# Kernel optimization log

Measured on AMD Instinct MI355X. Metric: run time of the kernel, lower is better.

The kernel has to match this reference:

```python
import jax, jax.numpy as jnp
import numpy as np

N = 200_000          # total nodes
C = 256              # in_channels
B = 64               # batch_size (num graphs)
NPG = N // B         # nodes per graph = max_num_nodes = 3125
E = 3_200_000        # edges (avg degree 16)
RATIO = 0.5
MULTIPLIER = 1.0


def setup_inputs() -> dict:
    key = jax.random.key(0)
    k1, k2, k3, k4, k5, k6 = jax.random.split(key, 6)
    x = jax.random.normal(k1, (N, C), dtype=jnp.float32)
    # hk.initializers.TruncatedNormal() ~ truncated normal, stddev 1
    p = jax.random.truncated_normal(k2, -2.0, 2.0, (C,), dtype=jnp.float32)
    # edges constrained within each graph (realistic graph batching)
    g = jax.random.randint(k3, (E,), 0, B, dtype=jnp.int32)
    senders = g * NPG + jax.random.randint(k4, (E,), 0, NPG, dtype=jnp.int32)
    receivers = g * NPG + jax.random.randint(k5, (E,), 0, NPG, dtype=jnp.int32)
    # sorted batch vector: graph id per node
    batch = jnp.arange(N, dtype=jnp.int32) // NPG
    return {"x": x, "p": p, "senders": senders, "receivers": receivers, "batch": batch}


def _segment_softmax(score, batch, num_segments):
    # batch_softmax from haiku-geometric: numerically-stable per-graph softmax
    mx = jax.ops.segment_max(score, batch, num_segments=num_segments)
    e = jnp.exp(score - mx[batch])
    denom = jax.ops.segment_sum(e, batch, num_segments=num_segments)
    return e / denom[batch]


def reference(x, p, senders, receivers, batch):
    batch_size = B
    num_nodes = x.shape[0]
    # per-node score: <x_i, p>, then softmax within each graph
    score = jnp.sum(x * p, axis=-1)                       # [N]
    score = _segment_softmax(score, batch, batch_size)    # [N]

    # select_batch_topk: keep first k nodes (by position) per graph,
    # move the rest to a new batch id == batch_size.
    nodes_per_batch = jax.ops.segment_sum(
        jnp.ones(num_nodes, dtype=jnp.int32), batch, num_segments=batch_size)
    cum_num_nodes = jnp.concatenate(
        [jnp.zeros(1, jnp.int32), jnp.cumsum(nodes_per_batch)[:-1].astype(jnp.int32)])
    # ratio < 1 branch
    k = jnp.ceil(RATIO * nodes_per_batch).astype(jnp.int32)   # [B]
    index_batch = jnp.arange(num_nodes, dtype=jnp.int32) - cum_num_nodes[batch]
    threshold_per_batch = k[batch] - 1
    new_batch = jnp.where(index_batch <= threshold_per_batch,
                          batch, jnp.full(batch.shape, batch_size, dtype=batch.dtype))

    # gate features by score (multiplier == 1 -> no extra scale)
    x_gated = x * score[:, None]

    # stable sort nodes so dropped nodes go to the end
    new_perm = jnp.argsort(new_batch)          # stable
    x_out = x_gated[new_perm]
    new_batch_sorted = new_batch[new_perm]

    # turn edges touching dropped nodes into self-loops (faithful to source,
    # including the sequential where-overwrite of senders then receivers)
    new_batch_idx = jnp.max(batch) + 1
    mask = (new_batch_sorted[senders] == new_batch_idx) | \
           (new_batch_sorted[receivers] == new_batch_idx)
    senders_out = jnp.where(mask, receivers, senders)
    receivers_out = jnp.where(mask, senders_out, receivers)
    return x_out, senders_out, receivers_out, new_batch_sorted
```

## Files before the change

### kernel.cpp

```cpp
#include <hip/hip_runtime.h>
#include <hip/hip_bf16.h>
#include <stdint.h>


#define RATIO 0.5f

typedef float f32x4 __attribute__((ext_vector_type(4)));
typedef int   i32x4 __attribute__((ext_vector_type(4)));

__global__ __launch_bounds__(256) void k_scores(
    const float* __restrict__ x, const float* __restrict__ p,
    float* __restrict__ s, int N) {
    int node = blockIdx.x * 4 + (threadIdx.x >> 6);
    int lane = threadIdx.x & 63;
    if (node >= N) return;
    const f32x4 pv = *reinterpret_cast<const f32x4*>(p + lane * 4);
    const f32x4 xv = *reinterpret_cast<const f32x4*>(x + (size_t)node * 256 + lane * 4);
    float acc = xv.x * pv.x + xv.y * pv.y + xv.z * pv.z + xv.w * pv.w;
    #pragma unroll
    for (int off = 32; off; off >>= 1) acc += __shfl_down(acc, off, 64);
    if (lane == 0) s[node] = acc;
}

__global__ __launch_bounds__(256) void k_boundary(
    const int* __restrict__ batch, int N, int* __restrict__ start) {
    int i = blockIdx.x * blockDim.x + threadIdx.x;
    if (i >= N) return;
    int b = batch[i];
    if (i == 0 || batch[i - 1] != b) start[b] = i;
}

__global__ __launch_bounds__(64) void k_meta(
    int N, int B, const int* __restrict__ start,
    int* __restrict__ kk, int* __restrict__ Kb, int* __restrict__ Db,
    int* __restrict__ Ktot) {
    int g = threadIdx.x;
    int st = start[g];
    int en = (g == B - 1) ? N : start[g + 1];
    int cnt = en - st;
    int kv = (int)ceilf(RATIO * (float)cnt);
    int dv = cnt - kv;
    int kp = kv, dp = dv;
    #pragma unroll
    for (int off = 1; off < 64; off <<= 1) {
        int a = __shfl_up(kp, off, 64);
        int b_ = __shfl_up(dp, off, 64);
        if (g >= off) { kp += a; dp += b_; }
    }
    kk[g] = kv;
    Kb[g] = kp - kv;
    Db[g] = dp - dv;
    if (g == B - 1) *Ktot = kp;
}

__global__ __launch_bounds__(256) void k_stats(
    const float* __restrict__ s, const int* __restrict__ start, int N, int B,
    float* __restrict__ mx, float* __restrict__ denom) {
    int g = blockIdx.x;
    int st = start[g];
    int en = (g == B - 1) ? N : start[g + 1];
    __shared__ float red[256];
    float m = -INFINITY;
    for (int i = st + threadIdx.x; i < en; i += 256) m = fmaxf(m, s[i]);
    red[threadIdx.x] = m; __syncthreads();
    for (int o = 128; o; o >>= 1) {
        if (threadIdx.x < o) red[threadIdx.x] = fmaxf(red[threadIdx.x], red[threadIdx.x + o]);
        __syncthreads();
    }
    m = red[0]; __syncthreads();
    float sum = 0.f;
    for (int i = st + threadIdx.x; i < en; i += 256) sum += expf(s[i] - m);
    red[threadIdx.x] = sum; __syncthreads();
    for (int o = 128; o; o >>= 1) {
        if (threadIdx.x < o) red[threadIdx.x] += red[threadIdx.x + o];
        __syncthreads();
    }
    if (threadIdx.x == 0) { mx[g] = m; denom[g] = red[0]; }
}

__global__ __launch_bounds__(256) void k_scatter(
    const float* __restrict__ x, const float* __restrict__ s,
    const int* __restrict__ batch, const int* __restrict__ start,
    const int* __restrict__ kk, const int* __restrict__ Kb, const int* __restrict__ Db,
    const int* __restrict__ Ktot, const float* __restrict__ mx, const float* __restrict__ denom,
    int N, int B, float* __restrict__ xout, float* __restrict__ nbout) {
    int node = blockIdx.x * 4 + (threadIdx.x >> 6);
    if (node >= N) return;
    int lane = threadIdx.x & 63;
    int g = batch[node];
    int idx = node - start[g];
    int kv = kk[g];
    bool kept = idx < kv;
    int pos = kept ? (Kb[g] + idx) : (*Ktot + Db[g] + (idx - kv));
    float sc = expf(s[node] - mx[g]) / denom[g];
    const f32x4 xv = *reinterpret_cast<const f32x4*>(x + (size_t)node * 256 + lane * 4);
    f32x4 o;
    o.x = xv.x * sc;
    o.y = xv.y * sc;
    o.z = xv.z * sc;
    o.w = xv.w * sc;
    __builtin_nontemporal_store(o, reinterpret_cast<f32x4*>(xout + (size_t)pos * 256 + lane * 4));
    if (lane == 0)
        __builtin_nontemporal_store((float)(kept ? g : B), nbout + pos);
}

__global__ __launch_bounds__(256) void k_edges(
    const int* __restrict__ snd, const int* __restrict__ rcv, int E,
    const int* __restrict__ Ktot,
    float* __restrict__ sout, float* __restrict__ rout) {
    int t = blockIdx.x * blockDim.x + threadIdx.x;
    int base = t * 4;
    if (base >= E) return;
    int kt = *Ktot;
    if (base + 4 <= E) {
        i32x4 s4 = __builtin_nontemporal_load(reinterpret_cast<const i32x4*>(snd + base));
        i32x4 r4 = __builtin_nontemporal_load(reinterpret_cast<const i32x4*>(rcv + base));
        f32x4 so, ro;
        so.x = (float)(((s4.x >= kt) || (r4.x >= kt)) ? r4.x : s4.x);
        so.y = (float)(((s4.y >= kt) || (r4.y >= kt)) ? r4.y : s4.y);
        so.z = (float)(((s4.z >= kt) || (r4.z >= kt)) ? r4.z : s4.z);
        so.w = (float)(((s4.w >= kt) || (r4.w >= kt)) ? r4.w : s4.w);
        ro.x = (float)r4.x;
        ro.y = (float)r4.y;
        ro.z = (float)r4.z;
        ro.w = (float)r4.w;
        __builtin_nontemporal_store(so, reinterpret_cast<f32x4*>(sout + base));
        __builtin_nontemporal_store(ro, reinterpret_cast<f32x4*>(rout + base));
    } else {
        for (int e = base; e < E; ++e) {
            int sv = snd[e], rv = rcv[e];
            bool m = (sv >= kt) || (rv >= kt);
            sout[e] = (float)(m ? rv : sv);
            rout[e] = (float)rv;
        }
    }
}

extern "C" void kernel_launch(void* const* d_in, const int* in_sizes, int n_in,
                              void* d_out, int out_size, void* d_ws, size_t ws_size,
                              hipStream_t stream) {
    const float* x = (const float*)d_in[0];
    const float* p = (const float*)d_in[1];
    const int* senders = (const int*)d_in[2];
    const int* receivers = (const int*)d_in[3];
    const int* batch = (const int*)d_in[4];

    const int C = in_sizes[1];
    const int E = in_sizes[2];
    const int N = in_sizes[4];
    const int B = 64;

    char* ws = (char*)d_ws;
    float* s   = (float*)ws;
    int* start = (int*)(ws + (size_t)N * 4);
    int* kk    = start + B;
    int* Kb    = kk + B;
    int* Db    = Kb + B;
    int* Ktot  = Db + B;
    float* mx    = (float*)(Ktot + 1);
    float* denom = mx + B;

    float* out   = (float*)d_out;
    float* xout  = out;
    float* sout  = out + (size_t)N * C;
    float* rout  = sout + E;
    float* nbout = rout + E;

    k_scores  <<<(N + 3) / 4, 256, 0, stream>>>(x, p, s, N);
    k_boundary<<<(N + 255) / 256, 256, 0, stream>>>(batch, N, start);
    k_meta    <<<1, 64, 0, stream>>>(N, B, start, kk, Kb, Db, Ktot);
    k_stats   <<<B, 256, 0, stream>>>(s, start, N, B, mx, denom);
    k_scatter <<<(N + 3) / 4, 256, 0, stream>>>(x, s, batch, start, kk, Kb, Db, Ktot,
                                                mx, denom, N, B, xout, nbout);
    k_edges   <<<(E + 1023) / 1024, 256, 0, stream>>>(senders, receivers, E, Ktot, sout, rout);
}
```

Baseline: 125.9 us.

## Fuse six kernels into three: scores+boundary, meta+stats, scatter+edges

Folds the graph-boundary detection into the score kernel and runs the prefix-sum metadata as an extra block of the softmax-stats kernel. The edge-remap work is piggybacked onto every estride-th block of the feature scatter kernel. This removes three kernel launches and their inter-kernel gaps, and lets the edge stream overlap the large feature copy. The cost is uneven work per block, since every sixteenth scatter block also handles an edge chunk.

```diff
diff --git a/kernel.cpp b/kernel.cpp
--- a/kernel.cpp
+++ b/kernel.cpp
@@ -8,9 +8,10 @@
 typedef float f32x4 __attribute__((ext_vector_type(4)));
 typedef int   i32x4 __attribute__((ext_vector_type(4)));
 
-__global__ __launch_bounds__(256) void k_scores(
+__global__ __launch_bounds__(256) void k1_scores_boundary(
     const float* __restrict__ x, const float* __restrict__ p,
-    float* __restrict__ s, int N) {
+    const int* __restrict__ batch,
+    float* __restrict__ s, int* __restrict__ start, int N) {
     int node = blockIdx.x * 4 + (threadIdx.x >> 6);
     int lane = threadIdx.x & 63;
     if (node >= N) return;
@@ -19,43 +20,38 @@
     float acc = xv.x * pv.x + xv.y * pv.y + xv.z * pv.z + xv.w * pv.w;
     #pragma unroll
     for (int off = 32; off; off >>= 1) acc += __shfl_down(acc, off, 64);
-    if (lane == 0) s[node] = acc;
+    if (lane == 0) {
+        s[node] = acc;
+        int b = batch[node];
+        if (node == 0 || batch[node - 1] != b) start[b] = node;
+    }
 }
 
-__global__ __launch_bounds__(256) void k_boundary(
-    const int* __restrict__ batch, int N, int* __restrict__ start) {
-    int i = blockIdx.x * blockDim.x + threadIdx.x;
-    if (i >= N) return;
-    int b = batch[i];
-    if (i == 0 || batch[i - 1] != b) start[b] = i;
-}
-
-__global__ __launch_bounds__(64) void k_meta(
-    int N, int B, const int* __restrict__ start,
+__global__ __launch_bounds__(256) void k2_meta_stats(
+    const float* __restrict__ s, const int* __restrict__ start, int N, int B,
     int* __restrict__ kk, int* __restrict__ Kb, int* __restrict__ Db,
-    int* __restrict__ Ktot) {
-    int g = threadIdx.x;
-    int st = start[g];
-    int en = (g == B - 1) ? N : start[g + 1];
-    int cnt = en - st;
-    int kv = (int)ceilf(RATIO * (float)cnt);
-    int dv = cnt - kv;
-    int kp = kv, dp = dv;
-    #pragma unroll
-    for (int off = 1; off < 64; off <<= 1) {
-        int a = __shfl_up(kp, off, 64);
-        int b_ = __shfl_up(dp, off, 64);
-        if (g >= off) { kp += a; dp += b_; }
+    int* __restrict__ Ktot, float* __restrict__ mx, float* __restrict__ denom) {
+    if (blockIdx.x == (unsigned)B) {
+        int g = threadIdx.x;
+        if (g >= B) return;
+        int st = start[g];
+        int en = (g == B - 1) ? N : start[g + 1];
+        int cnt = en - st;
+        int kv = (int)ceilf(RATIO * (float)cnt);
+        int dv = cnt - kv;
+        int kp = kv, dp = dv;
+        #pragma unroll
+        for (int off = 1; off < 64; off <<= 1) {
+            int a = __shfl_up(kp, off, 64);
+            int b_ = __shfl_up(dp, off, 64);
+            if (g >= off) { kp += a; dp += b_; }
+        }
+        kk[g] = kv;
+        Kb[g] = kp - kv;
+        Db[g] = dp - dv;
+        if (g == B - 1) *Ktot = kp;
+        return;
     }
-    kk[g] = kv;
-    Kb[g] = kp - kv;
-    Db[g] = dp - dv;
-    if (g == B - 1) *Ktot = kp;
-}
-
-__global__ __launch_bounds__(256) void k_stats(
-    const float* __restrict__ s, const int* __restrict__ start, int N, int B,
-    float* __restrict__ mx, float* __restrict__ denom) {
     int g = blockIdx.x;
     int st = start[g];
     int en = (g == B - 1) ? N : start[g + 1];
@@ -78,60 +74,60 @@
     if (threadIdx.x == 0) { mx[g] = m; denom[g] = red[0]; }
 }
 
-__global__ __launch_bounds__(256) void k_scatter(
+__global__ __launch_bounds__(256) void k3_scatter_edges(
     const float* __restrict__ x, const float* __restrict__ s,
     const int* __restrict__ batch, const int* __restrict__ start,
     const int* __restrict__ kk, const int* __restrict__ Kb, const int* __restrict__ Db,
     const int* __restrict__ Ktot, const float* __restrict__ mx, const float* __restrict__ denom,
-    int N, int B, float* __restrict__ xout, float* __restrict__ nbout) {
+    const int* __restrict__ snd, const int* __restrict__ rcv,
+    int N, int B, int E, int estride,
+    float* __restrict__ xout, float* __restrict__ nbout,
+    float* __restrict__ sout, float* __restrict__ rout) {
     int node = blockIdx.x * 4 + (threadIdx.x >> 6);
-    if (node >= N) return;
     int lane = threadIdx.x & 63;
-    int g = batch[node];
-    int idx = node - start[g];
-    int kv = kk[g];
-    bool kept = idx < kv;
-    int pos = kept ? (Kb[g] + idx) : (*Ktot + Db[g] + (idx - kv));
-    float sc = expf(s[node] - mx[g]) / denom[g];
-    const f32x4 xv = *reinterpret_cast<const f32x4*>(x + (size_t)node * 256 + lane * 4);
-    f32x4 o;
-    o.x = xv.x * sc;
-    o.y = xv.y * sc;
-    o.z = xv.z * sc;
-    o.w = xv.w * sc;
-    __builtin_nontemporal_store(o, reinterpret_cast<f32x4*>(xout + (size_t)pos * 256 + lane * 4));
-    if (lane == 0)
-        __builtin_nontemporal_store((float)(kept ? g : B), nbout + pos);
-}
-
-__global__ __launch_bounds__(256) void k_edges(
-    const int* __restrict__ snd, const int* __restrict__ rcv, int E,
-    const int* __restrict__ Ktot,
-    float* __restrict__ sout, float* __restrict__ rout) {
-    int t = blockIdx.x * blockDim.x + threadIdx.x;
-    int base = t * 4;
-    if (base >= E) return;
-    int kt = *Ktot;
-    if (base + 4 <= E) {
-        i32x4 s4 = __builtin_nontemporal_load(reinterpret_cast<const i32x4*>(snd + base));
-        i32x4 r4 = __builtin_nontemporal_load(reinterpret_cast<const i32x4*>(rcv + base));
-        f32x4 so, ro;
-        so.x = (float)(((s4.x >= kt) || (r4.x >= kt)) ? r4.x : s4.x);
-        so.y = (float)(((s4.y >= kt) || (r4.y >= kt)) ? r4.y : s4.y);
-        so.z = (float)(((s4.z >= kt) || (r4.z >= kt)) ? r4.z : s4.z);
-        so.w = (float)(((s4.w >= kt) || (r4.w >= kt)) ? r4.w : s4.w);
-        ro.x = (float)r4.x;
-        ro.y = (float)r4.y;
-        ro.z = (float)r4.z;
-        ro.w = (float)r4.w;
-        __builtin_nontemporal_store(so, reinterpret_cast<f32x4*>(sout + base));
-        __builtin_nontemporal_store(ro, reinterpret_cast<f32x4*>(rout + base));
-    } else {
-        for (int e = base; e < E; ++e) {
-            int sv = snd[e], rv = rcv[e];
-            bool m = (sv >= kt) || (rv >= kt);
-            sout[e] = (float)(m ? rv : sv);
-            rout[e] = (float)rv;
+    if (node < N) {
+        int g = batch[node];
+        int idx = node - start[g];
+        int kv = kk[g];
+        bool kept = idx < kv;
+        int pos = kept ? (Kb[g] + idx) : (*Ktot + Db[g] + (idx - kv));
+        float sc = expf(s[node] - mx[g]) / denom[g];
+        const f32x4 xv = *reinterpret_cast<const f32x4*>(x + (size_t)node * 256 + lane * 4);
+        f32x4 o;
+        o.x = xv.x * sc;
+        o.y = xv.y * sc;
+        o.z = xv.z * sc;
+        o.w = xv.w * sc;
+        __builtin_nontemporal_store(o, reinterpret_cast<f32x4*>(xout + (size_t)pos * 256 + lane * 4));
+        if (lane == 0)
+            __builtin_nontemporal_store((float)(kept ? g : B), nbout + pos);
+    }
+    if ((blockIdx.x % estride) == 0) {
+        long base = (long)(blockIdx.x / estride) * 1024 + threadIdx.x * 4;
+        if (base < E) {
+            int kt = *Ktot;
+            if (base + 4 <= E) {
+                i32x4 s4 = __builtin_nontemporal_load(reinterpret_cast<const i32x4*>(snd + base));
+                i32x4 r4 = __builtin_nontemporal_load(reinterpret_cast<const i32x4*>(rcv + base));
+                f32x4 so, ro;
+                so.x = (float)(((s4.x >= kt) || (r4.x >= kt)) ? r4.x : s4.x);
+                so.y = (float)(((s4.y >= kt) || (r4.y >= kt)) ? r4.y : s4.y);
+                so.z = (float)(((s4.z >= kt) || (r4.z >= kt)) ? r4.z : s4.z);
+                so.w = (float)(((s4.w >= kt) || (r4.w >= kt)) ? r4.w : s4.w);
+                ro.x = (float)r4.x;
+                ro.y = (float)r4.y;
+                ro.z = (float)r4.z;
+                ro.w = (float)r4.w;
+                __builtin_nontemporal_store(so, reinterpret_cast<f32x4*>(sout + base));
+                __builtin_nontemporal_store(ro, reinterpret_cast<f32x4*>(rout + base));
+            } else {
+                for (long e = base; e < E; ++e) {
+                    int sv = snd[e], rv = rcv[e];
+                    bool m = (sv >= kt) || (rv >= kt);
+                    sout[e] = (float)(m ? rv : sv);
+                    rout[e] = (float)rv;
+                }
+            }
         }
     }
 }
@@ -166,11 +162,14 @@
     float* rout  = sout + E;
     float* nbout = rout + E;
 
-    k_scores  <<<(N + 3) / 4, 256, 0, stream>>>(x, p, s, N);
-    k_boundary<<<(N + 255) / 256, 256, 0, stream>>>(batch, N, start);
-    k_meta    <<<1, 64, 0, stream>>>(N, B, start, kk, Kb, Db, Ktot);
-    k_stats   <<<B, 256, 0, stream>>>(s, start, N, B, mx, denom);
-    k_scatter <<<(N + 3) / 4, 256, 0, stream>>>(x, s, batch, start, kk, Kb, Db, Ktot,
-                                                mx, denom, N, B, xout, nbout);
-    k_edges   <<<(E + 1023) / 1024, 256, 0, stream>>>(senders, receivers, E, Ktot, sout, rout);
+    int grid = (N + 3) / 4;
+    int echunks = (E + 1023) / 1024;
+    int estride = grid / echunks; if (estride < 1) estride = 1;
+
+    k1_scores_boundary<<<grid, 256, 0, stream>>>(x, p, batch, s, start, N);
+    k2_meta_stats     <<<B + 1, 256, 0, stream>>>(s, start, N, B, kk, Kb, Db, Ktot, mx, denom);
+    k3_scatter_edges  <<<grid, 256, 0, stream>>>(x, s, batch, start, kk, Kb, Db, Ktot,
+                                                 mx, denom, senders, receivers,
+                                                 N, B, E, estride,
+                                                 xout, nbout, sout, rout);
 }
```

New measurement: 179.4 us. 1.42x slower.
